# Optimization experiments

Hardware: AMD Instinct MI355X
Metric: run time of the kernel (lower is better)

The kernel has to match this reference:

```python
import jax, jax.numpy as jnp
import numpy as np

B, L, D_MODEL = 2, 1024, 1024
D_STATE, D_CONV, EXPAND = 16, 4, 2
D_INNER = D_MODEL * EXPAND
LN_EPS = 1e-5


def setup_inputs() -> dict:
    key = jax.random.key(0)
    ks = jax.random.split(key, 6)
    g = lambda k, shape, scale: (jax.random.normal(k, shape, jnp.float32) * scale)
    x = jax.random.normal(ks[0], (B, L, D_MODEL), jnp.float32)
    in_proj_w = g(ks[1], (2 * D_INNER, D_MODEL), D_MODEL ** -0.5)
    conv_w = g(ks[2], (D_INNER, D_CONV), D_CONV ** -0.5)   # depthwise kernel
    conv_b = jnp.zeros((D_INNER,), jnp.float32)
    x_proj_w = g(ks[3], (2 * D_STATE + 1, D_INNER), D_INNER ** -0.5)
    A_log = jnp.tile(jnp.log(jnp.arange(1, D_STATE + 1, dtype=jnp.float32)), (D_INNER, 1))
    D_param = jnp.ones((D_INNER,), jnp.float32)
    dt_w = g(ks[4], (D_INNER, 1), 1.0)
    dt_b = jnp.full((D_INNER,), -4.0, jnp.float32)
    out_w = g(ks[5], (D_MODEL, D_INNER), D_INNER ** -0.5)
    ln_g = jnp.ones((D_INNER,), jnp.float32)
    ln_b = jnp.zeros((D_INNER,), jnp.float32)
    return dict(x=x, in_proj_w=in_proj_w, conv_w=conv_w, conv_b=conv_b,
                x_proj_w=x_proj_w, A_log=A_log, D_param=D_param,
                dt_w=dt_w, dt_b=dt_b, out_w=out_w, ln_g=ln_g, ln_b=ln_b)


def _forward(x, in_proj_w, conv_w, conv_b, x_proj_w, A_log, D_param,
             dt_w, dt_b, out_w, ln_g, ln_b):
    Lq = x.shape[1]
    xz = jnp.einsum('bld,ed->ble', x, in_proj_w)            # (B,L,2*Di)
    xb, z = xz[..., :D_INNER], xz[..., D_INNER:]
    # causal depthwise conv1d (pad left d_conv-1, valid conv == torch pad+truncate)
    xpad = jnp.pad(xb, ((0, 0), (D_CONV - 1, 0), (0, 0)))
    xc = conv_b
    for k in range(D_CONV):
        xc = xc + xpad[:, k:k + Lq, :] * conv_w[:, k]
    xb = jax.nn.silu(xc)
    proj = jnp.einsum('bld,ed->ble', xb, x_proj_w)          # (B,L,2N+1)
    dt_in = proj[..., :1]
    Bp = proj[..., 1:1 + D_STATE]                            # (B,L,N)
    Cp = proj[..., 1 + D_STATE:]                             # (B,L,N)
    dt = jax.nn.softplus(dt_in * dt_w[:, 0] + dt_b)          # (B,L,Di)
    A = -jnp.exp(A_log)                                      # (Di,N)
    dA = jnp.exp(dt[..., None] * A)                          # (B,L,Di,N)
    x_scaled = (xb * dt)[..., None] * Bp[..., None, :]       # (B,L,Di,N)
    # linear recurrence h[t] = dA[t]*h[t-1] + x_scaled[t] via associative scan
    def comb(a, b):
        return (a[0] * b[0], b[0] * a[1] + b[1])
    _, h = jax.lax.associative_scan(comb, (dA, x_scaled), axis=1)
    y = jnp.einsum('bldn,bln->bld', h, Cp) + xb * D_param    # (B,L,Di)
    mu = jnp.mean(y, axis=-1, keepdims=True)
    var = jnp.var(y, axis=-1, keepdims=True)
    y = (y - mu) / jnp.sqrt(var + LN_EPS) * ln_g + ln_b
    y = y * jax.nn.silu(z)
    return jnp.einsum('bld,ed->ble', y, out_w)               # (B,L,d_model)


def reference(x, in_proj_w, conv_w, conv_b, x_proj_w, A_log, D_param,
              dt_w, dt_b, out_w, ln_g, ln_b):
    return _forward(x, in_proj_w, conv_w, conv_b, x_proj_w, A_log, D_param,
                    dt_w, dt_b, out_w, ln_g, ln_b)
```

## Files before the change

### kernel.cpp

```cpp
#include <hip/hip_runtime.h>

typedef unsigned short u16;
typedef unsigned int u32;
typedef __bf16 bf16x8 __attribute__((ext_vector_type(8)));
typedef float f32x4 __attribute__((ext_vector_type(4)));
typedef unsigned short ushort8 __attribute__((ext_vector_type(8)));

__device__ __forceinline__ float bf2f(u16 b) {
    return __uint_as_float(((u32)b) << 16);
}
__device__ __forceinline__ u16 f2bf(float f) {
    u32 u = __float_as_uint(f);
    return (u16)((u + 0x7fffu + ((u >> 16) & 1u)) >> 16);
}

#define P_CONVW 0
#define P_CONVB 8192
#define P_ALOG  10240
#define P_DPAR  43008
#define P_DTW   45056
#define P_DTB   47104
#define P_LNG   49152
#define P_LNB   51200
#define P_TOTAL 53248

#define CCH 32
#define CT  32
#define CHUNKTOT 2097152
#define PSTRIDE 128

#define CV_X   524288
#define CV_W1  1572864
#define CV_TOT 2097152

struct ParamPtrs { const void* p[8]; };

__global__ __launch_bounds__(256) void canon_all(ParamPtrs pp, float* __restrict__ cpar,
                                                 const void* __restrict__ sx,
                                                 const void* __restrict__ sw1,
                                                 const void* __restrict__ swo,
                                                 u16* __restrict__ cx,
                                                 const void* __restrict__ sxp,
                                                 u16* __restrict__ wpad,
                                                 const u16* __restrict__ dp) {
    const bool isbf = (dp[0] != 0);
    const int blk = blockIdx.x;
    const int tid = threadIdx.x;
    if (blk < 8192) {
        const int i = blk * 256 + tid;
        const void* src;
        int off;
        if (i < CV_X)       { src = sx;  off = i; }
        else if (i < CV_W1) { src = sw1; off = i - CV_X; }
        else                { src = swo; off = i - CV_W1; }
        if (isbf) {
            ((uint2*)cx)[i] = ((const uint2*)src)[off];
        } else {
            const float4 v = ((const float4*)src)[off];
            uint2 o;
            o.x = (u32)f2bf(v.x) | ((u32)f2bf(v.y) << 16);
            o.y = (u32)f2bf(v.z) | ((u32)f2bf(v.w) << 16);
            ((uint2*)cx)[i] = o;
        }
    } else if (blk < 8400) {
        const int i = (blk - 8192) * 256 + tid;
        int seg, off;
        if (i < P_CONVB)      { seg = 0; off = i; }
        else if (i < P_ALOG)  { seg = 1; off = i - P_CONVB; }
        else if (i < P_DPAR)  { seg = 2; off = i - P_ALOG; }
        else if (i < P_DTW)   { seg = 3; off = i - P_DPAR; }
        else if (i < P_DTB)   { seg = 4; off = i - P_DTW; }
        else if (i < P_LNG)   { seg = 5; off = i - P_DTB; }
        else if (i < P_LNB)   { seg = 6; off = i - P_LNG; }
        else                  { seg = 7; off = i - P_LNB; }
        cpar[i] = isbf ? bf2f(((const u16*)pp.p[seg])[off]) : ((const float*)pp.p[seg])[off];
    } else {
        const int i = (blk - 8400) * 256 + tid;
        const int idx = i * 4;
        const int row = idx >> 11;
        u16 o[4];
#pragma unroll
        for (int q = 0; q < 4; ++q) {
            float v = 0.f;
            if (row < 33)
                v = isbf ? bf2f(((const u16*)sxp)[idx + q]) : ((const float*)sxp)[idx + q];
            o[q] = f2bf(v);
        }
        *(uint2*)&wpad[idx] = *(uint2*)o;
    }
}

__device__ __forceinline__ bf16x8 lds_frag(const char* smem, u32 base, int row, int kk,
                                           int quad, u32 xorv) {
    const u32 addr = (base + (u32)(row * 128 + kk * 64 + quad * 16)) ^ xorv;
    return *(const bf16x8*)(smem + addr);
}

template <int MODE>
__global__ __launch_bounds__(512, 2) void gemm8(const u16* __restrict__ A,
                                                const u16* __restrict__ Bw,
                                                void* __restrict__ C,
                                                int M, int N, int Kseg,
                                                int lda, int ldb) {
    extern __shared__ char smem[];
    const int bm = blockIdx.x, bn = blockIdx.y;
    const int kbase = blockIdx.z * Kseg;
    const int tid = threadIdx.x;
    const int lane = tid & 63, wave = tid >> 6;
    const int wm = wave >> 2, wn = wave & 3;
    const int l16 = lane & 15, quad = lane >> 4;
    const int NT = Kseg >> 6;
    const u32 xorv = (u32)((l16 & 7) << 4);

    const int rIss = wave * 8 + (lane >> 3);
    const int logC = (lane & 7) ^ ((lane >> 3) & 7);
    size_t aSrc[2], bSrc[4];
#pragma unroll
    for (int j = 0; j < 2; ++j)
        aSrc[j] = (size_t)(bm * 128 + j * 64 + rIss) * lda + logC * 8 + kbase;
#pragma unroll
    for (int j = 0; j < 4; ++j)
        bSrc[j] = (size_t)(bn * 256 + j * 64 + rIss) * ldb + logC * 8 + kbase;
    const u32 ldsW = (u32)(wave * 1024);

#define SG_A(slot, j, kel) __builtin_amdgcn_global_load_lds( \
        (const u32*)(A + aSrc[j] + (kel)), (u32*)(smem + (slot) + (j) * 8192 + ldsW), 16, 0, 0)
#define SG_B(slot, j, kel) __builtin_amdgcn_global_load_lds( \
        (const u32*)(Bw + bSrc[j] + (kel)), (u32*)(smem + (slot) + (j) * 8192 + ldsW), 16, 0, 0)

    const u32 sA0 = 0, sA1 = 16384, sA2 = 32768;
    const u32 sB0 = 49152, sB1 = 81920, sB2 = 114688;

    SG_A(sA0, 0, 0); SG_A(sA0, 1, 0);
    SG_B(sB0, 0, 0); SG_B(sB0, 1, 0); SG_B(sB0, 2, 0); SG_B(sB0, 3, 0);
    SG_A(sA1, 0, 64); SG_A(sA1, 1, 64);
    SG_B(sB1, 0, 64); SG_B(sB1, 1, 64); SG_B(sB1, 2, 64); SG_B(sB1, 3, 64);
    asm volatile("s_waitcnt vmcnt(6)" ::: "memory");
    __builtin_amdgcn_s_barrier();
    __builtin_amdgcn_sched_barrier(0);

    u32 curA = sA0, nxtA = sA1, stgA = sA2;
    u32 curB = sB0, nxtB = sB1, stgB = sB2;
    int kStage = 128;

    f32x4 acc[4][4] = {};
    bf16x8 a[4][2], b[4][2];

    for (int t = 0; t < NT; ++t) {
        const bool doStage = (t + 2) < NT;
#pragma unroll
        for (int mt = 0; mt < 4; ++mt)
#pragma unroll
            for (int kk = 0; kk < 2; ++kk)
                a[mt][kk] = lds_frag(smem, curA, wm * 64 + mt * 16 + l16, kk, quad, xorv);
#pragma unroll
        for (int nt = 0; nt < 2; ++nt)
#pragma unroll
            for (int kk = 0; kk < 2; ++kk)
                b[nt][kk] = lds_frag(smem, curB, wn * 64 + nt * 16 + l16, kk, quad, xorv);
        if (doStage) { SG_A(stgA, 0, kStage); SG_A(stgA, 1, kStage); SG_B(stgB, 0, kStage); }
        __builtin_amdgcn_s_setprio(1);
#pragma unroll
        for (int mt = 0; mt < 4; ++mt)
#pragma unroll
            for (int nt = 0; nt < 2; ++nt)
#pragma unroll
                for (int kk = 0; kk < 2; ++kk)
                    acc[mt][nt] = __builtin_amdgcn_mfma_f32_16x16x32_bf16(
                        a[mt][kk], b[nt][kk], acc[mt][nt], 0, 0, 0);
        __builtin_amdgcn_s_setprio(0);
#pragma unroll
        for (int nt = 2; nt < 4; ++nt)
#pragma unroll
            for (int kk = 0; kk < 2; ++kk)
                b[nt][kk] = lds_frag(smem, curB, wn * 64 + nt * 16 + l16, kk, quad, xorv);
        if (doStage) { SG_B(stgB, 1, kStage); SG_B(stgB, 2, kStage); SG_B(stgB, 3, kStage); }
        __builtin_amdgcn_s_setprio(1);
#pragma unroll
        for (int mt = 0; mt < 4; ++mt)
#pragma unroll
            for (int nt = 2; nt < 4; ++nt)
#pragma unroll
                for (int kk = 0; kk < 2; ++kk)
                    acc[mt][nt] = __builtin_amdgcn_mfma_f32_16x16x32_bf16(
                        a[mt][kk], b[nt][kk], acc[mt][nt], 0, 0, 0);
        __builtin_amdgcn_s_setprio(0);
        if (t < NT - 1) {
            if (doStage) asm volatile("s_waitcnt vmcnt(6)" ::: "memory");
            else         asm volatile("s_waitcnt vmcnt(0)" ::: "memory");
            __builtin_amdgcn_s_barrier();
            __builtin_amdgcn_sched_barrier(0);
            u32 tA = curA; curA = nxtA; nxtA = stgA; stgA = tA;
            u32 tB = curB; curB = nxtB; nxtB = stgB; stgB = tB;
            kStage += 64;
        }
    }
#undef SG_A
#undef SG_B

    float* Cf = (float*)C + (MODE == 1 ? (size_t)blockIdx.z * M * N : (size_t)0);
#pragma unroll
    for (int mt = 0; mt < 4; ++mt) {
#pragma unroll
        for (int r = 0; r < 4; ++r) {
            const int row = bm * 128 + wm * 64 + mt * 16 + quad * 4 + r;
#pragma unroll
            for (int nt = 0; nt < 4; ++nt) {
                const int col = bn * 256 + wn * 64 + nt * 16 + l16;
                if (MODE == 0)
                    ((u16*)C)[(size_t)row * N + col] = f2bf(acc[mt][nt][r]);
                else
                    Cf[(size_t)row * N + col] = acc[mt][nt][r];
            }
        }
    }
}

template <int MODE>
__global__ __launch_bounds__(256) void gemm_bt(const u16* __restrict__ A,
                                               const u16* __restrict__ Bw,
                                               void* __restrict__ C,
                                               int M, int N, int Kseg,
                                               int lda, int ldb) {
    const int bm = blockIdx.x;
    const int bn = blockIdx.y;
    const int kbase = blockIdx.z * Kseg;
    const int tid = threadIdx.x;
    const int lane = tid & 63;
    const int wave = tid >> 6;
    const int wm = wave >> 1, wn = wave & 1;
    const int l16 = lane & 15, quad = lane >> 4;

    __shared__ __align__(16) u16 sA[128 * 32];
    __shared__ __align__(16) u16 sB[128 * 32];

    f32x4 acc[4][4] = {};

    const int rsub = lane >> 2;
    const int csub = (lane & 3) * 8;

    for (int k0 = 0; k0 < Kseg; k0 += 32) {
        const int kc = kbase + k0 + csub;
        __syncthreads();
#pragma unroll
        for (int q = 0; q < 2; ++q) {
            const int g = wave + 4 * q;
            const int row = g * 16 + rsub;
            __builtin_amdgcn_global_load_lds(
                (const u32*)&A[(size_t)(bm * 128 + row) * lda + kc],
                (u32*)&sA[g * 512], 16, 0, 0);
            __builtin_amdgcn_global_load_lds(
                (const u32*)&Bw[(size_t)(bn * 128 + row) * ldb + kc],
                (u32*)&sB[g * 512], 16, 0, 0);
        }
        __syncthreads();

        bf16x8 af[4], bg[4];
#pragma unroll
        for (int t = 0; t < 4; ++t) {
            af[t] = *(const bf16x8*)&sA[(wm * 64 + t * 16 + l16) * 32 + quad * 8];
            bg[t] = *(const bf16x8*)&sB[(wn * 64 + t * 16 + l16) * 32 + quad * 8];
        }
#pragma unroll
        for (int mt = 0; mt < 4; ++mt)
#pragma unroll
            for (int nt = 0; nt < 4; ++nt)
                acc[mt][nt] = __builtin_amdgcn_mfma_f32_16x16x32_bf16(
                    af[mt], bg[nt], acc[mt][nt], 0, 0, 0);
    }

    float* Cf = (float*)C + (MODE == 1 ? (size_t)blockIdx.z * M * N : (size_t)0);
#pragma unroll
    for (int mt = 0; mt < 4; ++mt) {
#pragma unroll
        for (int r = 0; r < 4; ++r) {
            const int row = bm * 128 + wm * 64 + mt * 16 + quad * 4 + r;
#pragma unroll
            for (int nt = 0; nt < 4; ++nt) {
                const int col = bn * 128 + wn * 64 + nt * 16 + l16;
                if (MODE == 0)
                    ((u16*)C)[(size_t)row * N + col] = f2bf(acc[mt][nt][r]);
                else
                    Cf[(size_t)row * N + col] = acc[mt][nt][r];
            }
        }
    }
}

__global__ __launch_bounds__(256) void reduce_parts(const float* __restrict__ src,
                                                    float* __restrict__ dst,
                                                    int n4, int parts) {
    const int i = blockIdx.x * 256 + threadIdx.x;
    if (i >= n4) return;
    float4 s = ((const float4*)src)[i];
    for (int p = 1; p < parts; ++p) {
        const float4 v = ((const float4*)src)[(size_t)p * n4 + i];
        s.x += v.x; s.y += v.y; s.z += v.z; s.w += v.w;
    }
    ((float4*)dst)[i] = s;
}

__global__ __launch_bounds__(256) void conv_silu(const u16* __restrict__ xz,
                                                 const float* __restrict__ par,
                                                 u16* __restrict__ xb16) {
    const int idx = blockIdx.x * 256 + threadIdx.x;
    const int d8 = idx & 255;
    const int bl = idx >> 8;
    const int l = bl & 1023;
    const int d0 = d8 * 8;

    float acc[8];
    {
        const float4 b0 = *(const float4*)&par[P_CONVB + d0];
        const float4 b1 = *(const float4*)&par[P_CONVB + d0 + 4];
        acc[0] = b0.x; acc[1] = b0.y; acc[2] = b0.z; acc[3] = b0.w;
        acc[4] = b1.x; acc[5] = b1.y; acc[6] = b1.z; acc[7] = b1.w;
    }
    float warr[8][4];
#pragma unroll
    for (int q = 0; q < 8; ++q) {
        const float4 w = *(const float4*)&par[P_CONVW + (d0 + q) * 4];
        warr[q][0] = w.x; warr[q][1] = w.y; warr[q][2] = w.z; warr[q][3] = w.w;
    }
#pragma unroll
    for (int k = 0; k < 4; ++k) {
        const int ls = l + k - 3;
        if (ls >= 0) {
            const ushort8 xv = *(const ushort8*)&xz[(size_t)(bl + k - 3) * 4096 + d0];
#pragma unroll
            for (int q = 0; q < 8; ++q)
                acc[q] = fmaf(bf2f(xv[q]), warr[q][k], acc[q]);
        }
    }
    u16 o[8];
#pragma unroll
    for (int q = 0; q < 8; ++q) {
        const float s = acc[q] / (1.f + __expf(-acc[q]));
        o[q] = f2bf(s);
    }
    *(uint4*)&xb16[(size_t)bl * 2048 + d0] = *(uint4*)o;
}

__global__ __launch_bounds__(256) void scan_fused(const u16* __restrict__ xb16,
                                                  const float* __restrict__ proj,
                                                  const float* __restrict__ par,
                                                  u16* __restrict__ y) {
    const int tid = threadIdx.x;
    const int h2 = tid & 1;
    const int dsub = (tid >> 1) & 3;
    const int c = tid >> 3;
    const int d = blockIdx.x * 4 + dsub;
    const int b = blockIdx.z;
    const int nb = h2 * 8;

    __shared__ float Pl[CCH][4][17];
    __shared__ float Sl[CCH][4][17];

    float Aneg[8];
#pragma unroll
    for (int n = 0; n < 8; ++n) Aneg[n] = -__expf(par[P_ALOG + d * 16 + nb + n]);
    const float dtw = par[P_DTW + d], dtb = par[P_DTB + d];
    const float Dp = par[P_DPAR + d];

    const size_t row0 = (size_t)b * 1024 + (size_t)c * CT;

    {
        float hl[8] = {}, P[8];
#pragma unroll
        for (int n = 0; n < 8; ++n) P[n] = 1.f;
        float xv = bf2f(xb16[row0 * 2048 + d]);
        for (int i = 0; i < CT; ++i) {
            const float xv_next = (i + 1 < CT) ? bf2f(xb16[(row0 + i + 1) * 2048 + d]) : 0.f;
            const size_t pb = (row0 + i) * PSTRIDE;
            const float dtin = proj[pb];
            const float4 q0 = *(const float4*)&proj[pb + nb + 0];
            const float4 q1 = *(const float4*)&proj[pb + nb + 4];
            const float4 q2 = *(const float4*)&proj[pb + nb + 8];
            const float Bv[8] = {q0.y, q0.z, q0.w, q1.x, q1.y, q1.z, q1.w, q2.x};
            const float darg = fmaf(dtin, dtw, dtb);
            const float dt = (darg > 20.f) ? darg : __logf(1.f + __expf(darg));
            const float xdt = xv * dt;
#pragma unroll
            for (int n = 0; n < 8; ++n) {
                const float dA = __expf(dt * Aneg[n]);
                P[n] *= dA;
                hl[n] = fmaf(dA, hl[n], xdt * Bv[n]);
            }
            xv = xv_next;
        }
#pragma unroll
        for (int n = 0; n < 8; ++n) {
            Pl[c][dsub][nb + n] = P[n];
            Sl[c][dsub][nb + n] = hl[n];
        }
    }
    __syncthreads();

    if (tid < 64) {
        const int dd = tid >> 4, n = tid & 15;
        float hh = 0.f;
#pragma unroll
        for (int cc = 0; cc < CCH; ++cc) {
            const float p = Pl[cc][dd][n];
            const float s = Sl[cc][dd][n];
            Pl[cc][dd][n] = hh;
            hh = fmaf(p, hh, s);
        }
    }
    __syncthreads();

    {
        float hl[8];
#pragma unroll
        for (int n = 0; n < 8; ++n) hl[n] = Pl[c][dsub][nb + n];
        float xv = bf2f(xb16[row0 * 2048 + d]);
        for (int i = 0; i < CT; ++i) {
            const float xv_next = (i + 1 < CT) ? bf2f(xb16[(row0 + i + 1) * 2048 + d]) : 0.f;
            const size_t pb = (row0 + i) * PSTRIDE;
            const float dtin = proj[pb];
            const float4 q0 = *(const float4*)&proj[pb + nb + 0];
            const float4 q1 = *(const float4*)&proj[pb + nb + 4];
            const float4 q2 = *(const float4*)&proj[pb + nb + 8];
            const float4 r0 = *(const float4*)&proj[pb + 16 + nb + 0];
            const float4 r1 = *(const float4*)&proj[pb + 16 + nb + 4];
            const float4 r2 = *(const float4*)&proj[pb + 16 + nb + 8];
            const float Bv[8] = {q0.y, q0.z, q0.w, q1.x, q1.y, q1.z, q1.w, q2.x};
            const float Cv[8] = {r0.y, r0.z, r0.w, r1.x, r1.y, r1.z, r1.w, r2.x};
            const float darg = fmaf(dtin, dtw, dtb);
            const float dt = (darg > 20.f) ? darg : __logf(1.f + __expf(darg));
            const float xdt = xv * dt;
            float acc = 0.f;
#pragma unroll
            for (int n = 0; n < 8; ++n) {
                const float dA = __expf(dt * Aneg[n]);
                hl[n] = fmaf(dA, hl[n], xdt * Bv[n]);
                acc = fmaf(hl[n], Cv[n], acc);
            }
            acc += __shfl_xor(acc, 1);
            if (!h2)
                y[(row0 + i) * 2048 + d] = f2bf(fmaf(xv, Dp, acc));
            xv = xv_next;
        }
    }
}

__global__ __launch_bounds__(256) void ln_silu(const u16* __restrict__ y,
                                               const u16* __restrict__ xz,
                                               const float* __restrict__ par,
                                               u16* __restrict__ yn) {
    const int row = blockIdx.x;
    const int tid = threadIdx.x;
    const int lane = tid & 63, wave = tid >> 6;
    const int d0 = tid * 8;
    const ushort8 vy = *(const ushort8*)&y[(size_t)row * 2048 + d0];
    float v[8];
    float s = 0.f, s2 = 0.f;
#pragma unroll
    for (int i = 0; i < 8; ++i) {
        v[i] = bf2f(vy[i]);
        s += v[i];
        s2 = fmaf(v[i], v[i], s2);
    }
    s += __shfl_xor(s, 1); s2 += __shfl_xor(s2, 1);
    s += __shfl_xor(s, 2); s2 += __shfl_xor(s2, 2);
    s += __shfl_xor(s, 4); s2 += __shfl_xor(s2, 4);
    s += __shfl_xor(s, 8); s2 += __shfl_xor(s2, 8);
    s += __shfl_xor(s, 16); s2 += __shfl_xor(s2, 16);
    s += __shfl_xor(s, 32); s2 += __shfl_xor(s2, 32);
    __shared__ float rs[4], rs2[4];
    if (lane == 0) { rs[wave] = s; rs2[wave] = s2; }
    __syncthreads();
    const float ts = rs[0] + rs[1] + rs[2] + rs[3];
    const float ts2 = rs2[0] + rs2[1] + rs2[2] + rs2[3];
    const float mu = ts * (1.f / 2048.f);
    const float var = ts2 * (1.f / 2048.f) - mu * mu;
    const float rstd = rsqrtf(var + 1e-5f);

    const ushort8 vz = *(const ushort8*)&xz[(size_t)row * 4096 + 2048 + d0];
    float g[8], bb[8];
    {
        const float4 g0 = *(const float4*)&par[P_LNG + d0];
        const float4 g1 = *(const float4*)&par[P_LNG + d0 + 4];
        g[0] = g0.x; g[1] = g0.y; g[2] = g0.z; g[3] = g0.w;
        g[4] = g1.x; g[5] = g1.y; g[6] = g1.z; g[7] = g1.w;
        const float4 b0 = *(const float4*)&par[P_LNB + d0];
        const float4 b1 = *(const float4*)&par[P_LNB + d0 + 4];
        bb[0] = b0.x; bb[1] = b0.y; bb[2] = b0.z; bb[3] = b0.w;
        bb[4] = b1.x; bb[5] = b1.y; bb[6] = b1.z; bb[7] = b1.w;
    }
    u16 o[8];
#pragma unroll
    for (int i = 0; i < 8; ++i) {
        float t = (v[i] - mu) * rstd * g[i] + bb[i];
        const float z = bf2f(vz[i]);
        t *= z / (1.f + __expf(-z));
        o[i] = f2bf(t);
    }
    *(uint4*)&yn[(size_t)row * 2048 + d0] = *(uint4*)o;
}

extern "C" void kernel_launch(void* const* d_in, const int* in_sizes, int n_in,
                              void* d_out, int out_size, void* d_ws, size_t ws_size,
                              hipStream_t stream) {
    const void* x         = d_in[0];
    const void* in_proj_w = d_in[1];
    const void* conv_w    = d_in[2];
    const void* conv_b    = d_in[3];
    const void* x_proj_w  = d_in[4];
    const void* A_log     = d_in[5];
    const void* D_param   = d_in[6];
    const void* dt_w      = d_in[7];
    const void* dt_b      = d_in[8];
    const void* out_w     = d_in[9];
    const void* ln_g      = d_in[10];
    const void* ln_b      = d_in[11];
    const u16* dp = (const u16*)D_param;

    float* cpar = (float*)d_ws;
    u16* cx     = (u16*)(cpar + P_TOTAL);
    u16* cw1    = cx + 2097152;
    u16* cwo    = cw1 + 4194304;
    u16* xz     = cwo + 2097152;
    u16* xb16   = xz + 8388608;
    u16* y      = xb16 + 4194304;
    u16* wpad   = y + 4194304;
    float* proj = (float*)(wpad + 262144);
    float* PS   = proj + 262144;
    float* H    = PS + 2 * CHUNKTOT;
    float* gpart = H + CHUNKTOT;
    float* xpart = gpart;
    u16* yn      = xb16;

    static bool attrSet = false;
    if (!attrSet) {
        hipFuncSetAttribute(reinterpret_cast<const void*>(&gemm8<0>),
                            hipFuncAttributeMaxDynamicSharedMemorySize, 147456);
        hipFuncSetAttribute(reinterpret_cast<const void*>(&gemm8<1>),
                            hipFuncAttributeMaxDynamicSharedMemorySize, 147456);
        attrSet = true;
    }

    ParamPtrs pp;
    pp.p[0] = conv_w; pp.p[1] = conv_b; pp.p[2] = A_log; pp.p[3] = D_param;
    pp.p[4] = dt_w;   pp.p[5] = dt_b;   pp.p[6] = ln_g;  pp.p[7] = ln_b;
    canon_all<<<8656, 256, 0, stream>>>(pp, cpar, x, in_proj_w, out_w, cx,
                                        x_proj_w, wpad, dp);

    gemm8<0><<<dim3(16, 16, 1), 512, 147456, stream>>>(cx, cw1, xz,
                                                       2048, 4096, 1024, 1024, 1024);
    conv_silu<<<2048, 256, 0, stream>>>(xz, cpar, xb16);
    gemm_bt<1><<<dim3(16, 1, 16), 256, 0, stream>>>(xb16, wpad, xpart, 2048, 128, 128, 2048, 2048);
    reduce_parts<<<256, 256, 0, stream>>>(xpart, proj, 65536, 16);
    scan_fused<<<dim3(512, 1, 2), 256, 0, stream>>>(xb16, proj, cpar, y);
    ln_silu<<<2048, 256, 0, stream>>>(y, xz, cpar, yn);
    gemm8<1><<<dim3(16, 4, 2), 512, 147456, stream>>>(yn, cwo, gpart,
                                                      2048, 1024, 1024, 2048, 2048);
    reduce_parts<<<2048, 256, 0, stream>>>(gpart, (float*)d_out, 524288, 2);
}
```

Baseline: 233.3 us.

## Stage proj rows through shared memory with register prefetch in scan kernel

The scan kernel now loads each chunk's proj rows cooperatively, one float4 per thread, into a shared-memory buffer in batches of four timesteps, prefetching the next batch into registers while the current one is computed. This replaces the redundant per-thread global float4 loads of B and C. The chunk decay product is also computed once as exp(sum(dt)*A) instead of a running product of per-step decays. The cost is two block-wide barriers per batch and extra shared memory, which may limit occupancy.

New measurement: 289.5 us. +24.1%, slower.

```diff
diff --git a/kernel.cpp b/kernel.cpp
--- a/kernel.cpp
+++ b/kernel.cpp
@@ -341,18 +341,23 @@
     *(uint4*)&xb16[(size_t)bl * 2048 + d0] = *(uint4*)o;
 }
 
+#define SPS 148
+#define SBATCH 4
+
 __global__ __launch_bounds__(256) void scan_fused(const u16* __restrict__ xb16,
                                                   const float* __restrict__ proj,
                                                   const float* __restrict__ par,
                                                   u16* __restrict__ y) {
     const int tid = threadIdx.x;
-    const int h2 = tid & 1;
+    const int half = tid & 1;
     const int dsub = (tid >> 1) & 3;
     const int c = tid >> 3;
+    const int q = tid & 7;
     const int d = blockIdx.x * 4 + dsub;
     const int b = blockIdx.z;
-    const int nb = h2 * 8;
-
+    const int nb = half * 8;
+
+    __shared__ float sp[32 * SPS];
     __shared__ float Pl[CCH][4][17];
     __shared__ float Sl[CCH][4][17];
 
@@ -362,37 +367,77 @@
     const float dtw = par[P_DTW + d], dtb = par[P_DTB + d];
     const float Dp = par[P_DPAR + d];
 
-    const size_t row0 = (size_t)b * 1024 + (size_t)c * CT;
-
-    {
-        float hl[8] = {}, P[8];
-#pragma unroll
-        for (int n = 0; n < 8; ++n) P[n] = 1.f;
-        float xv = bf2f(xb16[row0 * 2048 + d]);
-        for (int i = 0; i < CT; ++i) {
-            const float xv_next = (i + 1 < CT) ? bf2f(xb16[(row0 + i + 1) * 2048 + d]) : 0.f;
-            const size_t pb = (row0 + i) * PSTRIDE;
-            const float dtin = proj[pb];
-            const float4 q0 = *(const float4*)&proj[pb + nb + 0];
-            const float4 q1 = *(const float4*)&proj[pb + nb + 4];
-            const float4 q2 = *(const float4*)&proj[pb + nb + 8];
+    const size_t rowc = (size_t)b * 1024 + (size_t)c * CT;
+
+    float4 stg[SBATCH];
+    float stg32[SBATCH];
+
+#pragma unroll
+    for (int ii = 0; ii < SBATCH; ++ii)
+        stg[ii] = *(const float4*)(proj + (rowc + ii) * PSTRIDE + q * 4);
+    if (q == 0) {
+#pragma unroll
+        for (int ii = 0; ii < SBATCH; ++ii)
+            stg32[ii] = proj[(rowc + ii) * PSTRIDE + 32];
+    }
+
+    float hl[8] = {};
+    float dtsum = 0.f;
+    for (int i0 = 0; i0 < CT; i0 += SBATCH) {
+        __syncthreads();
+#pragma unroll
+        for (int ii = 0; ii < SBATCH; ++ii)
+            *(float4*)&sp[c * SPS + ii * 36 + q * 4] = stg[ii];
+        if (q == 0) {
+#pragma unroll
+            for (int ii = 0; ii < SBATCH; ++ii)
+                sp[c * SPS + ii * 36 + 32] = stg32[ii];
+        }
+        if (i0 + SBATCH < CT) {
+#pragma unroll
+            for (int ii = 0; ii < SBATCH; ++ii)
+                stg[ii] = *(const float4*)(proj + (rowc + i0 + SBATCH + ii) * PSTRIDE + q * 4);
+            if (q == 0) {
+#pragma unroll
+                for (int ii = 0; ii < SBATCH; ++ii)
+                    stg32[ii] = proj[(rowc + i0 + SBATCH + ii) * PSTRIDE + 32];
+            }
+        }
+        __syncthreads();
+#pragma unroll
+        for (int ii = 0; ii < SBATCH; ++ii) {
+            const int i = i0 + ii;
+            const float* rp = &sp[c * SPS + ii * 36];
+            const float dtin = rp[0];
+            const float4 q0 = *(const float4*)(rp + nb);
+            const float4 q1 = *(const float4*)(rp + nb + 4);
+            const float4 q2 = *(const float4*)(rp + nb + 8);
             const float Bv[8] = {q0.y, q0.z, q0.w, q1.x, q1.y, q1.z, q1.w, q2.x};
+            const float xv = bf2f(xb16[(rowc + i) * 2048 + d]);
             const float darg = fmaf(dtin, dtw, dtb);
             const float dt = (darg > 20.f) ? darg : __logf(1.f + __expf(darg));
+            dtsum += dt;
             const float xdt = xv * dt;
 #pragma unroll
             for (int n = 0; n < 8; ++n) {
                 const float dA = __expf(dt * Aneg[n]);
-                P[n] *= dA;
                 hl[n] = fmaf(dA, hl[n], xdt * Bv[n]);
             }
-            xv = xv_next;
-        }
-#pragma unroll
-        for (int n = 0; n < 8; ++n) {
-            Pl[c][dsub][nb + n] = P[n];
-            Sl[c][dsub][nb + n] = hl[n];
-        }
+        }
+    }
+#pragma unroll
+    for (int n = 0; n < 8; ++n) {
+        Pl[c][dsub][nb + n] = __expf(dtsum * Aneg[n]);
+        Sl[c][dsub][nb + n] = hl[n];
+    }
+
+#pragma unroll
+    for (int ii = 0; ii < SBATCH; ++ii)
+        stg[ii] = *(const float4*)(proj + (rowc + ii) * PSTRIDE + q * 4);
+    if (q == 0) {
+#pragma unroll
+        for (int ii = 0; ii < SBATCH; ++ii)
+            stg32[ii] = proj[(rowc + ii) * PSTRIDE + 32];
     }
     __syncthreads();
 
@@ -409,23 +454,43 @@
     }
     __syncthreads();
 
-    {
-        float hl[8];
-#pragma unroll
-        for (int n = 0; n < 8; ++n) hl[n] = Pl[c][dsub][nb + n];
-        float xv = bf2f(xb16[row0 * 2048 + d]);
-        for (int i = 0; i < CT; ++i) {
-            const float xv_next = (i + 1 < CT) ? bf2f(xb16[(row0 + i + 1) * 2048 + d]) : 0.f;
-            const size_t pb = (row0 + i) * PSTRIDE;
-            const float dtin = proj[pb];
-            const float4 q0 = *(const float4*)&proj[pb + nb + 0];
-            const float4 q1 = *(const float4*)&proj[pb + nb + 4];
-            const float4 q2 = *(const float4*)&proj[pb + nb + 8];
-            const float4 r0 = *(const float4*)&proj[pb + 16 + nb + 0];
-            const float4 r1 = *(const float4*)&proj[pb + 16 + nb + 4];
-            const float4 r2 = *(const float4*)&proj[pb + 16 + nb + 8];
+#pragma unroll
+    for (int n = 0; n < 8; ++n) hl[n] = Pl[c][dsub][nb + n];
+    for (int i0 = 0; i0 < CT; i0 += SBATCH) {
+        __syncthreads();
+#pragma unroll
+        for (int ii = 0; ii < SBATCH; ++ii)
+            *(float4*)&sp[c * SPS + ii * 36 + q * 4] = stg[ii];
+        if (q == 0) {
+#pragma unroll
+            for (int ii = 0; ii < SBATCH; ++ii)
+                sp[c * SPS + ii * 36 + 32] = stg32[ii];
+        }
+        if (i0 + SBATCH < CT) {
+#pragma unroll
+            for (int ii = 0; ii < SBATCH; ++ii)
+                stg[ii] = *(const float4*)(proj + (rowc + i0 + SBATCH + ii) * PSTRIDE + q * 4);
+            if (q == 0) {
+#pragma unroll
+                for (int ii = 0; ii < SBATCH; ++ii)
+                    stg32[ii] = proj[(rowc + i0 + SBATCH + ii) * PSTRIDE + 32];
+            }
+        }
+        __syncthreads();
+#pragma unroll
+        for (int ii = 0; ii < SBATCH; ++ii) {
+            const int i = i0 + ii;
+            const float* rp = &sp[c * SPS + ii * 36];
+            const float dtin = rp[0];
+            const float4 q0 = *(const float4*)(rp + nb);
+            const float4 q1 = *(const float4*)(rp + nb + 4);
+            const float4 q2 = *(const float4*)(rp + nb + 8);
+            const float4 r0 = *(const float4*)(rp + 16 + nb);
+            const float4 r1 = *(const float4*)(rp + 20 + nb);
+            const float4 r2 = *(const float4*)(rp + 24 + nb);
             const float Bv[8] = {q0.y, q0.z, q0.w, q1.x, q1.y, q1.z, q1.w, q2.x};
             const float Cv[8] = {r0.y, r0.z, r0.w, r1.x, r1.y, r1.z, r1.w, r2.x};
+            const float xv = bf2f(xb16[(rowc + i) * 2048 + d]);
             const float darg = fmaf(dtin, dtw, dtb);
             const float dt = (darg > 20.f) ? darg : __logf(1.f + __expf(darg));
             const float xdt = xv * dt;
@@ -437,9 +502,8 @@
                 acc = fmaf(hl[n], Cv[n], acc);
             }
             acc += __shfl_xor(acc, 1);
-            if (!h2)
-                y[(row0 + i) * 2048 + d] = f2bf(fmaf(xv, Dp, acc));
-            xv = xv_next;
+            if (!half)
+                y[(rowc + i) * 2048 + d] = f2bf(fmaf(xv, Dp, acc));
         }
     }
 }
```
